# Kernel optimization log

Measured on AMD Instinct MI355X. Metric: run time of the kernel, lower is better.

## Reference

```python
import jax, jax.numpy as jnp
import numpy as np

EPS = 1e-8


def decode_fcos_obb(loc, deltas):
    """FCOS-style OBB decode. deltas = (d_x-, d_y-, d_z-, d_x+, d_y+, d_z+, theta):
    distances from the point to the 6 box faces, measured in the box's yaw-rotated
    frame. Returns OBB (x, y, z, w, l, h, theta)."""
    theta = deltas[:, 6]
    w = deltas[:, 0] + deltas[:, 3]
    l = deltas[:, 1] + deltas[:, 4]
    h = deltas[:, 2] + deltas[:, 5]
    ox = (deltas[:, 3] - deltas[:, 0]) * 0.5
    oy = (deltas[:, 4] - deltas[:, 1]) * 0.5
    oz = (deltas[:, 5] - deltas[:, 2]) * 0.5
    c, s = jnp.cos(theta), jnp.sin(theta)
    cx = loc[:, 0] + ox * c - oy * s
    cy = loc[:, 1] + ox * s + oy * c
    cz = loc[:, 2] + oz
    return jnp.stack([cx, cy, cz, w, l, h, theta], axis=-1)


def box2corners(box):
    # box: (B,N,5) = (x,y,w,h,alpha) -> (B,N,4,2) CCW corners
    x, y, w, h, a = (box[..., i] for i in range(5))
    x4 = jnp.asarray([0.5, -0.5, -0.5, 0.5], box.dtype) * w[..., None]
    y4 = jnp.asarray([0.5, 0.5, -0.5, -0.5], box.dtype) * h[..., None]
    c, s = jnp.cos(a)[..., None], jnp.sin(a)[..., None]
    return jnp.stack([x4 * c - y4 * s + x[..., None],
                      x4 * s + y4 * c + y[..., None]], axis=-1)


def box_intersection(corners1, corners2):
    # Pairwise intersections of the 4 edges of box1 with the 4 edges of box2.
    # Returns points (B,N,4,4,2) and validity mask (B,N,4,4).
    l1 = jnp.concatenate([corners1, jnp.roll(corners1, -1, axis=2)], axis=-1)[:, :, :, None, :]
    l2 = jnp.concatenate([corners2, jnp.roll(corners2, -1, axis=2)], axis=-1)[:, :, None, :, :]
    x1, y1, x2, y2 = l1[..., 0], l1[..., 1], l1[..., 2], l1[..., 3]
    x3, y3, x4, y4 = l2[..., 0], l2[..., 1], l2[..., 2], l2[..., 3]
    num = (y4 - y3) * (x2 - x1) - (x4 - x3) * (y2 - y1)
    den_t = (x4 - x3) * (y1 - y3) - (y4 - y3) * (x1 - x3)
    den_u = (x2 - x1) * (y1 - y3) - (y2 - y1) * (x1 - x3)
    safe = jnp.where(num == 0., 1., num)
    t = jnp.where(num == 0., -1., den_t / safe)
    u = jnp.where(num == 0., -1., -den_u / safe)
    mask = (t > 0.) & (t < 1.) & (u > 0.) & (u < 1.)
    t2 = den_t / (num + EPS)
    pts = jnp.stack([x1 + t2 * (x2 - x1), y1 + t2 * (y2 - y1)], axis=-1)
    pts = pts * mask[..., None].astype(pts.dtype)
    return pts, mask


def box1_in_box2(corners1, corners2):
    # Which corners of box1 lie inside box2 (projection onto box2's edge frame).
    a = corners2[:, :, 0:1, :]
    b = corners2[:, :, 1:2, :]
    d = corners2[:, :, 3:4, :]
    ab, ad, am = b - a, d - a, corners1 - a
    p_ab = (ab * am).sum(-1) / (ab * ab).sum(-1)
    p_ad = (ad * am).sum(-1) / (ad * ad).sum(-1)
    tol = 1e-6
    return (p_ab > -tol) & (p_ab < 1 + tol) & (p_ad > -tol) & (p_ad < 1 + tol)


def sorted_polygon_area(vertices, mask):
    # vertices: (B,N,24,2) candidate polygon vertices, mask: (B,N,24) validity.
    # Sort valid vertices CCW around their centroid, pad with the first vertex,
    # shoelace area. Equivalent to Rotated_IoU's sort_vertices + calculate_area.
    m = mask.astype(vertices.dtype)
    nv = m.sum(-1)  # (B,N) number of valid vertices
    mean = (vertices * m[..., None]).sum(2) / jnp.maximum(nv, 1.)[..., None]
    v = vertices - mean[:, :, None, :]
    ang = jnp.where(mask, jnp.arctan2(v[..., 1], v[..., 0]), 1e6)  # invalid -> last
    idx = jnp.argsort(ang, axis=-1)
    vs = jnp.take_along_axis(v, idx[..., None], axis=2)
    pos = jnp.arange(vertices.shape[2])
    pad = pos[None, None, :] >= nv[..., None]
    vs = jnp.where(pad[..., None], vs[:, :, :1, :], vs)  # pad with first valid vertex
    nxt = jnp.roll(vs, -1, axis=2)
    cross = vs[..., 0] * nxt[..., 1] - vs[..., 1] * nxt[..., 0]
    return 0.5 * jnp.abs(cross.sum(-1))


def cal_iou(box1, box2):
    c1 = box2corners(box1)
    c2 = box2corners(box2)
    pts, m_i = box_intersection(c1, c2)
    B, N = box1.shape[:2]
    vertices = jnp.concatenate([c1, c2, pts.reshape(B, N, 16, 2)], axis=2)
    mask = jnp.concatenate([box1_in_box2(c1, c2), box1_in_box2(c2, c1),
                            m_i.reshape(B, N, 16)], axis=2)
    inter = sorted_polygon_area(vertices, mask)
    u = box1[..., 2] * box1[..., 3] + box2[..., 2] * box2[..., 3] - inter
    return inter / u, u


def cal_iou_3d(b1, b2):
    # boxes: (B,N,7) = (x,y,z,w,l,h,theta); 2D rotated IoU in xy, overlap in z.
    box1 = jnp.stack([b1[..., 0], b1[..., 1], b1[..., 3], b1[..., 4], b1[..., 6]], -1)
    box2 = jnp.stack([b2[..., 0], b2[..., 1], b2[..., 3], b2[..., 4], b2[..., 6]], -1)
    zmax1, zmin1 = b1[..., 2] + b1[..., 5] * 0.5, b1[..., 2] - b1[..., 5] * 0.5
    zmax2, zmin2 = b2[..., 2] + b2[..., 5] * 0.5, b2[..., 2] - b2[..., 5] * 0.5
    z_overlap = jnp.clip(jnp.minimum(zmax1, zmax2) - jnp.maximum(zmin1, zmin2), 0.)
    iou_2d, u = cal_iou(box1, box2)
    inter_3d = iou_2d * u * z_overlap
    v1 = b1[..., 3] * b1[..., 4] * b1[..., 5]
    v2 = b2[..., 3] * b2[..., 4] * b2[..., 5]
    u3d = v1 + v2 - inter_3d
    return inter_3d / u3d, u3d


def rotated_iou_loss(pred, target, weight):
    loc = jnp.zeros((pred.shape[0], 3), pred.dtype)
    pb = decode_fcos_obb(loc, pred)[None]     # (1,N,7)
    tb = decode_fcos_obb(loc, target)[None]   # (1,N,7)
    ious, unions = cal_iou_3d(pb, tb)
    vol_inter = ious * unions
    ious = (vol_inter + 1.0) / (unions + 1.0)  # smoothed IoU
    losses = -jnp.log(ious)
    return (losses * weight).sum()


def setup_inputs():
    key = jax.random.key(0)
    k1, k2, k3 = jax.random.split(key, 3)
    N = 250000

    def make_deltas(k):
        u = jax.random.uniform(k, (N, 7), dtype=jnp.float32)
        dists = u[:, :6] * 2.0 + 0.3               # positive face distances
        theta = (u[:, 6:7] - 0.5) * jnp.pi          # yaw in (-pi/2, pi/2)
        return jnp.concatenate([dists, theta], axis=1)

    return {
        "pred": make_deltas(k1),
        "target": make_deltas(k2),
        "weight": jax.random.uniform(k3, (N,), dtype=jnp.float32),
    }


def reference(pred, target, weight):
    return rotated_iou_loss(pred, target, weight)
```

## Files before the change

kernel.cpp:

```cpp
#include <hip/hip_runtime.h>
#include <math.h>


#define RCP(x) __builtin_amdgcn_rcpf(x)

typedef _Float16 half2v __attribute__((ext_vector_type(2)));

#define ACCC(M, X, Y, CID) { float f_ = (M) ? 1.0f : 0.0f; \
    sx##CID = fmaf(f_, (X), sx##CID); \
    sy##CID = fmaf(f_, (Y), sy##CID); \
    nv##CID += f_; }

#define PIB_B(MX, MY, M) { float amx = (MX) - c2x0, amy = (MY) - c2y0; \
        float pab = (f0x * amx + f0y * amy) * rabB; \
        float pdd = (adxB * amx + adyB * amy) * radB; \
        M = (fabsf(pab - 0.5f) < HT) & (fabsf(pdd - 0.5f) < HT); }
#define PIB_A(MX, MY, M) { float amx = (MX) - c1x0, amy = (MY) - c1y0; \
        float pab = (e0x * amx + e0y * amy) * rabA; \
        float pdd = (adxA * amx + adyA * amy) * radA; \
        M = (fabsf(pab - 0.5f) < HT) & (fabsf(pdd - 0.5f) < HT); }

#define ISECT(X1, Y1, EX, EY, X3, Y3, FX, FY, RR, PX, PY, MM, FF) { \
        float gx_ = (X1) - (X3), gy_ = (Y1) - (Y3); \
        float dt_ = (FX) * gy_ - (FY) * gx_; \
        float du_ = (EX) * gy_ - (EY) * gx_; \
        float tt_ = dt_ * (RR), uu_ = -du_ * (RR); \
        MM = (fabsf(tt_ - 0.5f) < 0.5f) & (fabsf(uu_ - 0.5f) < 0.5f); \
        FF = (MM) ? 1.0f : 0.0f; \
        PX = (X1) + tt_ * (EX); PY = (Y1) + tt_ * (EY); }

#define EDGE_GROUP(X1, Y1, EX, EY, R0, R1, R2, R3, OX0, OY0, OX1, OY1, MO0, MO1, CID) { \
        float pax, pay, pbx, pby, pcx, pcy, pdx, pdy; \
        float fa, fb, fc, fd; bool ma, mb, mc, md; \
        ISECT(X1, Y1, EX, EY, c2x0, c2y0, f0x, f0y, R0, pax, pay, ma, fa) \
        ISECT(X1, Y1, EX, EY, c2x1, c2y1, f1x, f1y, R1, pbx, pby, mb, fb) \
        ISECT(X1, Y1, EX, EY, c2x2, c2y2, f2x, f2y, R2, pcx, pcy, mc, fc) \
        ISECT(X1, Y1, EX, EY, c2x3, c2y3, f3x, f3y, R3, pdx, pdy, md, fd) \
        sx##CID += ((ma ? pax : 0.0f) + (mb ? pbx : 0.0f)) \
                 + ((mc ? pcx : 0.0f) + (md ? pdx : 0.0f)); \
        sy##CID += ((ma ? pay : 0.0f) + (mb ? pby : 0.0f)) \
                 + ((mc ? pcy : 0.0f) + (md ? pdy : 0.0f)); \
        float gcf_ = (fa + fb) + (fc + fd); \
        nv##CID += gcf_; \
        MO0 = gcf_ > 0.5f; MO1 = gcf_ > 1.5f; \
        float cdx_ = mc ? pcx : pdx,  cdy_ = mc ? pcy : pdy; \
        float bcx_ = mb ? pbx : cdx_, bcy_ = mb ? pby : cdy_; \
        OX0 = ma ? pax : bcx_;        OY0 = ma ? pay : bcy_; \
        float s2x_ = mb ? cdx_ : pdx, s2y_ = mb ? cdy_ : pdy; \
        OX1 = ma ? bcx_ : s2x_;       OY1 = ma ? bcy_ : s2y_; }

#define ANGPACK(K) { float xc = vx##K - mx_, yc = vy##K - my_; \
        float tt = xc * RCP(fmaxf(fabsf(xc) + fabsf(yc), 1e-38f)); \
        float key = copysignf(1.0f - tt, yc); \
        ang##K = m##K ? key : 1e6f; \
        pk##K = __builtin_bit_cast(unsigned, __builtin_amdgcn_cvt_pkrtz(xc, yc)); }
#define CE(A, B) { bool sw = ang##A > ang##B; \
        float mn = fminf(ang##A, ang##B), mx2 = fmaxf(ang##A, ang##B); \
        ang##A = mn; ang##B = mx2; \
        unsigned ta = pk##A; pk##A = sw ? pk##B : pk##A; pk##B = sw ? ta : pk##B; }
#define PAD(K) { pk##K = (ang##K > 5e5f) ? pk0 : pk##K; }
#define UPX(K) float ux##K, uy##K; { half2v h_ = __builtin_bit_cast(half2v, pk##K); \
        ux##K = (float)h_.x; uy##K = (float)h_.y; }
#define SHOE(A, B, C) { cs##C = fmaf(ux##A, uy##B, cs##C); \
                        cs##C = fmaf(-uy##A, ux##B, cs##C); }

__device__ __forceinline__ float riou_item(
    const float* __restrict__ pred, const float* __restrict__ tgt, float wg, int idx)
{
    const float* pp = pred + 7 * idx;
    const float* qq = tgt + 7 * idx;
    float p0 = pp[0], p1 = pp[1], p2 = pp[2], p3 = pp[3], p4 = pp[4], p5 = pp[5], p6 = pp[6];
    float q0 = qq[0], q1 = qq[1], q2 = qq[2], q3 = qq[3], q4 = qq[4], q5 = qq[5], q6 = qq[6];

    float w1 = p0 + p3, l1 = p1 + p4, h1 = p2 + p5;
    float oz1 = (p5 - p2) * 0.5f;
    float ox1 = (p3 - p0) * 0.5f, oy1 = (p4 - p1) * 0.5f;
    float sA, cA; __sincosf(p6, &sA, &cA);
    float cx1 = ox1 * cA - oy1 * sA, cy1 = ox1 * sA + oy1 * cA;

    float w2 = q0 + q3, l2 = q1 + q4, h2 = q2 + q5;
    float oz2 = (q5 - q2) * 0.5f;
    float ox2 = (q3 - q0) * 0.5f, oy2 = (q4 - q1) * 0.5f;
    float sB, cB; __sincosf(q6, &sB, &cB);
    float cx2 = ox2 * cB - oy2 * sB, cy2 = ox2 * sB + oy2 * cB;

    float vol1 = w1 * l1 * h1, vol2 = w2 * l2 * h2;
    float zo = fmaxf(fminf(oz1 + h1 * 0.5f, oz2 + h2 * 0.5f) -
                     fmaxf(oz1 - h1 * 0.5f, oz2 - h2 * 0.5f), 0.0f);

    float hw1 = 0.5f * w1, hl1 = 0.5f * l1;
    float c1x0 =  hw1 * cA - hl1 * sA + cx1, c1y0 =  hw1 * sA + hl1 * cA + cy1;
    float c1x1 = -hw1 * cA - hl1 * sA + cx1, c1y1 = -hw1 * sA + hl1 * cA + cy1;
    float c1x2 = -hw1 * cA + hl1 * sA + cx1, c1y2 = -hw1 * sA - hl1 * cA + cy1;
    float c1x3 =  hw1 * cA + hl1 * sA + cx1, c1y3 =  hw1 * sA - hl1 * cA + cy1;
    float hw2 = 0.5f * w2, hl2 = 0.5f * l2;
    float c2x0 =  hw2 * cB - hl2 * sB + cx2, c2y0 =  hw2 * sB + hl2 * cB + cy2;
    float c2x1 = -hw2 * cB - hl2 * sB + cx2, c2y1 = -hw2 * sB + hl2 * cB + cy2;
    float c2x2 = -hw2 * cB + hl2 * sB + cx2, c2y2 = -hw2 * sB - hl2 * cB + cy2;
    float c2x3 =  hw2 * cB + hl2 * sB + cx2, c2y3 =  hw2 * sB - hl2 * cB + cy2;

    float e0x = c1x1 - c1x0, e0y = c1y1 - c1y0;
    float e1x = c1x2 - c1x1, e1y = c1y2 - c1y1;
    float e2x = c1x3 - c1x2, e2y = c1y3 - c1y2;
    float e3x = c1x0 - c1x3, e3y = c1y0 - c1y3;
    float f0x = c2x1 - c2x0, f0y = c2y1 - c2y0;
    float f1x = c2x2 - c2x1, f1y = c2y2 - c2y1;
    float f2x = c2x3 - c2x2, f2y = c2y3 - c2y2;
    float f3x = c2x0 - c2x3, f3y = c2y0 - c2y3;

    float sx0 = 0.f, sx1 = 0.f, sx2 = 0.f, sx3 = 0.f;
    float sy0 = 0.f, sy1 = 0.f, sy2 = 0.f, sy3 = 0.f;
    float nv0 = 0.f, nv1 = 0.f, nv2 = 0.f, nv3 = 0.f;

    const float HT = 0.5f + 1e-6f;
    float adxB = c2x3 - c2x0, adyB = c2y3 - c2y0;
    float rabB = RCP(w2 * w2), radB = RCP(l2 * l2);
    bool mA0, mA1, mA2, mA3;
    PIB_B(c1x0, c1y0, mA0) PIB_B(c1x1, c1y1, mA1)
    PIB_B(c1x2, c1y2, mA2) PIB_B(c1x3, c1y3, mA3)
    ACCC(mA0, c1x0, c1y0, 0) ACCC(mA1, c1x1, c1y1, 1)
    ACCC(mA2, c1x2, c1y2, 2) ACCC(mA3, c1x3, c1y3, 3)
    float adxA = c1x3 - c1x0, adyA = c1y3 - c1y0;
    float rabA = RCP(w1 * w1), radA = RCP(l1 * l1);
    bool mB0, mB1, mB2, mB3;
    PIB_A(c2x0, c2y0, mB0) PIB_A(c2x1, c2y1, mB1)
    PIB_A(c2x2, c2y2, mB2) PIB_A(c2x3, c2y3, mB3)
    ACCC(mB0, c2x0, c2y0, 0) ACCC(mB1, c2x1, c2y1, 1)
    ACCC(mB2, c2x2, c2y2, 2) ACCC(mB3, c2x3, c2y3, 3)

    float r00 = RCP(f0y * e0x - f0x * e0y);
    float r01 = RCP(f1y * e0x - f1x * e0y);
    float r10 = RCP(f0y * e1x - f0x * e1y);
    float r11 = RCP(f1y * e1x - f1x * e1y);

    bool m8, m9, m10, m11, m12, m13, m14, m15;
    float vx8, vy8, vx9, vy9, vx10, vy10, vx11, vy11;
    float vx12, vy12, vx13, vy13, vx14, vy14, vx15, vy15;
    EDGE_GROUP(c1x0, c1y0, e0x, e0y,  r00,  r01, -r00, -r01,
               vx8,  vy8,  vx9,  vy9,  m8,  m9,  0)
    EDGE_GROUP(c1x1, c1y1, e1x, e1y,  r10,  r11, -r10, -r11,
               vx10, vy10, vx11, vy11, m10, m11, 1)
    EDGE_GROUP(c1x2, c1y2, e2x, e2y, -r00, -r01,  r00,  r01,
               vx12, vy12, vx13, vy13, m12, m13, 2)
    EDGE_GROUP(c1x3, c1y3, e3x, e3y, -r10, -r11,  r10,  r11,
               vx14, vy14, vx15, vy15, m14, m15, 3)

    float vx0 = c1x0, vy0 = c1y0, vx1 = c1x1, vy1 = c1y1;
    float vx2 = c1x2, vy2 = c1y2, vx3 = c1x3, vy3 = c1y3;
    float vx4 = c2x0, vy4 = c2y0, vx5 = c2x1, vy5 = c2y1;
    float vx6 = c2x2, vy6 = c2y2, vx7 = c2x3, vy7 = c2y3;
    bool m0 = mA0, m1 = mA1, m2 = mA2, m3 = mA3;
    bool m4 = mB0, m5 = mB1, m6 = mB2, m7 = mB3;

    float nv = (nv0 + nv1) + (nv2 + nv3);
    float inv_nv = RCP(fmaxf(nv, 1.0f));
    float mx_ = ((sx0 + sx1) + (sx2 + sx3)) * inv_nv;
    float my_ = ((sy0 + sy1) + (sy2 + sy3)) * inv_nv;
    float ang0, ang1, ang2, ang3, ang4, ang5, ang6, ang7;
    float ang8, ang9, ang10, ang11, ang12, ang13, ang14, ang15;
    unsigned pk0, pk1, pk2, pk3, pk4, pk5, pk6, pk7;
    unsigned pk8, pk9, pk10, pk11, pk12, pk13, pk14, pk15;
    ANGPACK(0) ANGPACK(1) ANGPACK(2) ANGPACK(3)
    ANGPACK(4) ANGPACK(5) ANGPACK(6) ANGPACK(7)
    ANGPACK(8) ANGPACK(9) ANGPACK(10) ANGPACK(11)
    ANGPACK(12) ANGPACK(13) ANGPACK(14) ANGPACK(15)

    CE(0,1) CE(2,3) CE(4,5) CE(6,7) CE(8,9) CE(10,11) CE(12,13) CE(14,15)
    CE(0,2) CE(1,3) CE(4,6) CE(5,7) CE(8,10) CE(9,11) CE(12,14) CE(13,15)
    CE(1,2) CE(5,6) CE(9,10) CE(13,14)
    CE(0,4) CE(1,5) CE(2,6) CE(3,7) CE(8,12) CE(9,13) CE(10,14) CE(11,15)
    CE(2,4) CE(3,5) CE(10,12) CE(11,13)
    CE(1,2) CE(3,4) CE(5,6) CE(9,10) CE(11,12) CE(13,14)
    CE(0,8) CE(1,9) CE(2,10) CE(3,11) CE(4,12) CE(5,13) CE(6,14) CE(7,15)
    CE(4,8) CE(5,9) CE(6,10) CE(7,11)
    CE(2,4) CE(3,5) CE(6,8) CE(7,9) CE(10,12) CE(11,13)
    CE(1,2) CE(3,4) CE(5,6) CE(7,8) CE(9,10) CE(11,12) CE(13,14)

    PAD(1) PAD(2) PAD(3) PAD(4) PAD(5) PAD(6) PAD(7) PAD(8)
    PAD(9) PAD(10) PAD(11) PAD(12) PAD(13) PAD(14) PAD(15)

    UPX(0) UPX(1) UPX(2) UPX(3) UPX(4) UPX(5) UPX(6) UPX(7)
    UPX(8) UPX(9) UPX(10) UPX(11) UPX(12) UPX(13) UPX(14) UPX(15)
    float cs0 = 0.f, cs1 = 0.f, cs2 = 0.f, cs3 = 0.f;
    SHOE(0,1,0)  SHOE(1,2,0)  SHOE(2,3,0)   SHOE(3,4,0)
    SHOE(4,5,1)  SHOE(5,6,1)  SHOE(6,7,1)   SHOE(7,8,1)
    SHOE(8,9,2)  SHOE(9,10,2) SHOE(10,11,2) SHOE(11,12,2)
    SHOE(12,13,3) SHOE(13,14,3) SHOE(14,15,3) SHOE(15,0,3)
    float cs = (cs0 + cs1) + (cs2 + cs3);
    float inter = 0.5f * fabsf(cs);

    float inter3d = inter * zo;
    float u3d = vol1 + vol2 - inter3d;
    float iouf = (inter3d + 1.0f) * RCP(u3d + 1.0f);
    return -__logf(iouf) * wg;
}

__global__ __launch_bounds__(256, 4) void riou_loss_kernel(
    const float* __restrict__ pred, const float* __restrict__ tgt,
    const float* __restrict__ wgt, float* __restrict__ ws, int n)
{
    int i0 = blockIdx.x * 256 + threadIdx.x;
    int idx0 = min(i0, n - 1);
    float wg0 = (i0 < n) ? wgt[idx0] : 0.0f;
    float loss = riou_item(pred, tgt, wg0, idx0);

#pragma unroll
    for (int off = 32; off > 0; off >>= 1)
        loss += __shfl_down(loss, off, 64);
    __shared__ float wsum[4];
    int lane = threadIdx.x & 63, wid = threadIdx.x >> 6;
    if (lane == 0) wsum[wid] = loss;
    __syncthreads();
    if (threadIdx.x == 0)
        ws[blockIdx.x] = wsum[0] + wsum[1] + wsum[2] + wsum[3];
}

__global__ __launch_bounds__(256) void riou_reduce_kernel(
    const float* __restrict__ ws, float* __restrict__ out, int nb)
{
    float s = 0.0f;
    for (int t = threadIdx.x; t < nb; t += 256) s += ws[t];
#pragma unroll
    for (int off = 32; off > 0; off >>= 1)
        s += __shfl_down(s, off, 64);
    __shared__ float wsum[4];
    int lane = threadIdx.x & 63, wid = threadIdx.x >> 6;
    if (lane == 0) wsum[wid] = s;
    __syncthreads();
    if (threadIdx.x == 0)
        out[0] = wsum[0] + wsum[1] + wsum[2] + wsum[3];
}

extern "C" void kernel_launch(void* const* d_in, const int* in_sizes, int n_in,
                              void* d_out, int out_size, void* d_ws, size_t ws_size,
                              hipStream_t stream) {
    const float* pred = (const float*)d_in[0];
    const float* tgt  = (const float*)d_in[1];
    const float* wgt  = (const float*)d_in[2];
    float* out = (float*)d_out;
    float* ws  = (float*)d_ws;
    int n = in_sizes[2];

    int grid = (n + 255) / 256;
    riou_loss_kernel<<<grid, 256, 0, stream>>>(pred, tgt, wgt, ws, n);
    riou_reduce_kernel<<<1, 256, 0, stream>>>(ws, out, grid);
}
```

Measured before the change: 74.14 us.

## Fuse final reduction into main kernel via last-block atomic counters

Removes the separate reduction kernel launch. Each block writes its partial sum to workspace, and a two-level atomic counter (8 sharded counters plus a super counter) picks the last-finishing block to do the final sum. A memset of the counters is added each call, and launch bounds drop from 4 to 2 waves per SIMD, which changes register allocation. The atomic exchange with an inline-asm data dependency is there to order the partial write before the counter increment without a full fence, which is fragile with respect to memory ordering.

```diff
diff --git a/kernel.cpp b/kernel.cpp
--- a/kernel.cpp
+++ b/kernel.cpp
@@ -195,9 +195,11 @@
     return -__logf(iouf) * wg;
 }
 
-__global__ __launch_bounds__(256, 4) void riou_loss_kernel(
+
+__global__ __launch_bounds__(256, 2) void riou_loss_kernel(
     const float* __restrict__ pred, const float* __restrict__ tgt,
-    const float* __restrict__ wgt, float* __restrict__ ws, int n)
+    const float* __restrict__ wgt, float* __restrict__ out,
+    float* __restrict__ ws, int n)
 {
     int i0 = blockIdx.x * 256 + threadIdx.x;
     int idx0 = min(i0, n - 1);
@@ -208,27 +210,50 @@
     for (int off = 32; off > 0; off >>= 1)
         loss += __shfl_down(loss, off, 64);
     __shared__ float wsum[4];
+    __shared__ int isfin;
     int lane = threadIdx.x & 63, wid = threadIdx.x >> 6;
     if (lane == 0) wsum[wid] = loss;
     __syncthreads();
-    if (threadIdx.x == 0)
-        ws[blockIdx.x] = wsum[0] + wsum[1] + wsum[2] + wsum[3];
-}
-
-__global__ __launch_bounds__(256) void riou_reduce_kernel(
-    const float* __restrict__ ws, float* __restrict__ out, int nb)
-{
-    float s = 0.0f;
-    for (int t = threadIdx.x; t < nb; t += 256) s += ws[t];
+
+    int* cnt8  = (int*)ws;
+    int* super = (int*)ws + 256;
+    float* part = ws + 512;
+    int nb = gridDim.x;
+
+    if (threadIdx.x == 0) {
+        float partial = wsum[0] + wsum[1] + wsum[2] + wsum[3];
+        float old = __hip_atomic_exchange(&part[blockIdx.x], partial,
+                        __ATOMIC_RELAXED, __HIP_MEMORY_SCOPE_AGENT);
+        unsigned z;
+        asm volatile("v_and_b32 %0, 0, %1"
+                     : "=v"(z) : "v"(__float_as_int(old)));
+        int r = blockIdx.x & 7;
+        int tgt_r = (nb + 7 - r) >> 3;
+        int c = __hip_atomic_fetch_add(&cnt8[r * 32], 1 + (int)z,
+                        __ATOMIC_RELAXED, __HIP_MEMORY_SCOPE_AGENT);
+        int fin = 0;
+        if (c == tgt_r - 1) {
+            int s = __hip_atomic_fetch_add(super, 1,
+                        __ATOMIC_RELAXED, __HIP_MEMORY_SCOPE_AGENT);
+            fin = (s == min(nb, 8) - 1);
+        }
+        isfin = fin;
+    }
+    __syncthreads();
+
+    if (isfin) {
+        float s = 0.0f;
+        for (int t = threadIdx.x; t < nb; t += 256)
+            s += __hip_atomic_load(&part[t], __ATOMIC_RELAXED,
+                                   __HIP_MEMORY_SCOPE_AGENT);
 #pragma unroll
-    for (int off = 32; off > 0; off >>= 1)
-        s += __shfl_down(s, off, 64);
-    __shared__ float wsum[4];
-    int lane = threadIdx.x & 63, wid = threadIdx.x >> 6;
-    if (lane == 0) wsum[wid] = s;
-    __syncthreads();
-    if (threadIdx.x == 0)
-        out[0] = wsum[0] + wsum[1] + wsum[2] + wsum[3];
+        for (int off = 32; off > 0; off >>= 1)
+            s += __shfl_down(s, off, 64);
+        if (lane == 0) wsum[wid] = s;
+        __syncthreads();
+        if (threadIdx.x == 0)
+            out[0] = wsum[0] + wsum[1] + wsum[2] + wsum[3];
+    }
 }
 
 extern "C" void kernel_launch(void* const* d_in, const int* in_sizes, int n_in,
@@ -241,7 +266,7 @@
     float* ws  = (float*)d_ws;
     int n = in_sizes[2];
 
+    hipMemsetAsync(d_ws, 0, 2048, stream);
     int grid = (n + 255) / 256;
-    riou_loss_kernel<<<grid, 256, 0, stream>>>(pred, tgt, wgt, ws, n);
-    riou_reduce_kernel<<<1, 256, 0, stream>>>(ws, out, grid);
+    riou_loss_kernel<<<grid, 256, 0, stream>>>(pred, tgt, wgt, out, ws, n);
 }
```

After: 76.64 us. +3.4%, slower.
